# Kernel optimization log

Measured on AMD Instinct MI355X. Metric: run time of the kernel, lower is better.

## Reference

```python
import jax, jax.numpy as jnp
import numpy as np

D_MODEL = 512
N_HEADS = 12
EPS = 1e-5
_DIM = D_MODEL // N_HEADS          # 42
_REM = D_MODEL % N_HEADS           # 8
HEAD_DIMS = [_DIM + 1 if i < _REM else _DIM for i in range(N_HEADS)]  # sums to 512


def _layernorm(x, gamma, beta):
    mu = jnp.mean(x, axis=-1, keepdims=True)
    var = jnp.mean((x - mu) ** 2, axis=-1, keepdims=True)
    return (x - mu) * jax.lax.rsqrt(var + EPS) * gamma + beta


def setup_inputs() -> dict:
    key = jax.random.key(0)
    ks = jax.random.split(key, 12)
    S, B, D = 2048, 16, D_MODEL
    sc = 0.02
    return {
        "x":   jax.random.normal(ks[0], (S, B, D), jnp.float32),
        "Wq":  jax.random.normal(ks[1], (D, D), jnp.float32) * sc,
        "Wk":  jax.random.normal(ks[2], (D, D), jnp.float32) * sc,
        "Wv":  jax.random.normal(ks[3], (D, D), jnp.float32) * sc,
        "g1":  jnp.ones((D,), jnp.float32),
        "b1":  jnp.zeros((D,), jnp.float32),
        "g2":  jnp.ones((D,), jnp.float32),
        "b2":  jnp.zeros((D,), jnp.float32),
        "W_ffn1": jax.random.normal(ks[4], (D, D), jnp.float32) * sc,
        "b_ffn1": jnp.zeros((D,), jnp.float32),
        "W_ffn2": jax.random.normal(ks[5], (D, D), jnp.float32) * sc,
        "b_ffn2": jnp.zeros((D,), jnp.float32),
    }


def reference(x, Wq, Wk, Wv, g1, b1, g2, b2, W_ffn1, b_ffn1, W_ffn2, b_ffn2):
    # x: [S, B, D]; attention over S, batched over B (per source transpose [1,0,2])
    normed = _layernorm(x, g1, b1)
    q = jnp.transpose(normed @ Wq, (1, 0, 2))  # [B, S, D]
    k = jnp.transpose(normed @ Wk, (1, 0, 2))
    v = jnp.transpose(normed @ Wv, (1, 0, 2))

    outs = []
    idx = 0
    for hd in HEAD_DIMS:  # fixed small loop over structurally-distinct head dims
        q_i = q[:, :, idx:idx + hd]
        k_i = k[:, :, idx:idx + hd]
        v_i = v[:, :, idx:idx + hd]
        scores = jnp.einsum('bsd,btd->bst', q_i, k_i) / np.float32(np.sqrt(hd))
        attn = jax.nn.softmax(scores, axis=-1)  # dropout off (inference)
        outs.append(jnp.transpose(attn @ v_i, (1, 0, 2)))  # back to [S, B, hd]
        idx += hd

    attn_out = _layernorm(jnp.concatenate(outs, axis=-1) + x, g2, b2)
    ffn = jax.nn.relu(attn_out @ W_ffn1 + b_ffn1) @ W_ffn2 + b_ffn2
    return attn_out + ffn
```

## Files before the change

### kernel.cpp

```cpp
#include <hip/hip_runtime.h>
#include <hip/hip_bf16.h>


#define M_ROWS 32768
#define DM 512
#define SEQ 2048
#define BATCH 16
#define SLAB_ELEMS (24u * 1024u * 1024u)

typedef __bf16 bf16x8 __attribute__((ext_vector_type(8)));
typedef float f32x4 __attribute__((ext_vector_type(4)));
typedef float f32x16 __attribute__((ext_vector_type(16)));

#define EXP2F(x) __builtin_amdgcn_exp2f(x)

typedef __attribute__((address_space(3))) unsigned lds_u32;
typedef __attribute__((address_space(1))) unsigned glb_u32;
#define GL2LDS(src, dst) __builtin_amdgcn_global_load_lds( \
    (const glb_u32*)(const void*)(src), (lds_u32*)(void*)(dst), 16, 0, 0)

#define BARRIER_VM4() asm volatile("s_waitcnt vmcnt(4)\ns_barrier" ::: "memory")
#define BARRIER_VM2() asm volatile("s_waitcnt vmcnt(2)\ns_barrier" ::: "memory")
#define BARRIER_VM0() asm volatile("s_waitcnt vmcnt(0)\ns_barrier" ::: "memory")
#define BARRIER_ONLY() asm volatile("s_barrier" ::: "memory")

#define MFMA16(a, b, c) __builtin_amdgcn_mfma_f32_16x16x32_bf16(a, b, c, 0, 0, 0)

__device__ inline unsigned pkbf16(float a, float b) {
    unsigned r;
    asm("v_cvt_pk_bf16_f32 %0, %1, %2" : "=v"(r) : "v"(a), "v"(b));
    return r;
}

__global__ __launch_bounds__(256) void prep_kernel(
    const float* __restrict__ Wq, const float* __restrict__ Wk,
    const float* __restrict__ Wv, const float* __restrict__ Wf1,
    const float* __restrict__ Wf2, __bf16* __restrict__ Wts,
    __bf16* __restrict__ q, __bf16* __restrict__ v,
    const float* __restrict__ x, const float* __restrict__ g1,
    const float* __restrict__ b1, __bf16* __restrict__ normed)
{
    int blk = blockIdx.x;
    if (blk < 5120) {
        int g = blk >> 10;
        int idx = (blk & 1023) * 256 + threadIdx.x;
        const float* W = (g == 0) ? Wq : (g == 1) ? Wk : (g == 2) ? Wv
                        : (g == 3) ? Wf1 : Wf2;
        __bf16* Wt = Wts + (size_t)g * (DM * DM);
        int n = idx >> 9, k = idx & 511;
        Wt[idx] = (__bf16)W[k * DM + n];
    } else if (blk < 6656) {
        int row = (blk - 5120) * 256 + threadIdx.x;
        union { __bf16 h[8]; bf16x8 v8; } z;
#pragma unroll
        for (int j = 0; j < 8; ++j) z.h[j] = (__bf16)0.f;
        *(bf16x8*)(q + (size_t)row * 64 + 40) = z.v8;
    } else if (blk < 6848) {
        int i = (blk - 6656) * 256 + threadIdx.x;
        int bh = i >> 8, s8 = i & 255;
        int hd = ((bh % 12) < 8) ? 43 : 42;
        union { __bf16 h[8]; bf16x8 v8; } o;
#pragma unroll
        for (int j = 0; j < 8; ++j) o.h[j] = (__bf16)1.0f;
        *(bf16x8*)(v + ((size_t)bh * 64 + hd) * SEQ + s8 * 8) = o.v8;
    } else {
        int wid  = (int)(((blk - 6848) * 256 + threadIdx.x) >> 6);
        int lane = threadIdx.x & 63;
        int bb = wid >> 11, ss = wid & 2047;
        const float* xrow = x + ((size_t)ss * 16 + bb) * DM;
        float vv[8];
        *(float4*)&vv[0] = *(const float4*)(xrow + lane * 8);
        *(float4*)&vv[4] = *(const float4*)(xrow + lane * 8 + 4);
        float s = 0.f, sq = 0.f;
#pragma unroll
        for (int j = 0; j < 8; ++j) { s += vv[j]; sq = fmaf(vv[j], vv[j], sq); }
#pragma unroll
        for (int i = 1; i < 64; i <<= 1) { s += __shfl_xor(s, i); sq += __shfl_xor(sq, i); }
        float mu   = s * (1.0f / 512.0f);
        float var  = sq * (1.0f / 512.0f) - mu * mu;
        float rstd = rsqrtf(var + 1e-5f);
        union { __bf16 h[8]; bf16x8 v8; } o;
#pragma unroll
        for (int j = 0; j < 8; ++j)
            o.h[j] = (__bf16)((vv[j] - mu) * rstd * g1[lane * 8 + j] + b1[lane * 8 + j]);
        *(bf16x8*)(normed + (size_t)wid * DM + lane * 8) = o.v8;
    }
}

__global__ __launch_bounds__(256) void ln2_kernel(
    const __bf16* __restrict__ in, const float* __restrict__ res,
    const float* __restrict__ g, const float* __restrict__ b,
    __bf16* __restrict__ outb)
{
    int wid  = (int)((blockIdx.x * 256 + threadIdx.x) >> 6);
    int lane = threadIdx.x & 63;
    int bb = wid >> 11, ss = wid & 2047;
    union { __bf16 h[8]; bf16x8 v8; } iv;
    iv.v8 = *(const bf16x8*)(in + (size_t)wid * DM + lane * 8);
    const float* rrow = res + ((size_t)ss * 16 + bb) * DM;
    float v[8];
    float4 r0 = *(const float4*)(rrow + lane * 8);
    float4 r1 = *(const float4*)(rrow + lane * 8 + 4);
    v[0] = (float)iv.h[0] + r0.x; v[1] = (float)iv.h[1] + r0.y;
    v[2] = (float)iv.h[2] + r0.z; v[3] = (float)iv.h[3] + r0.w;
    v[4] = (float)iv.h[4] + r1.x; v[5] = (float)iv.h[5] + r1.y;
    v[6] = (float)iv.h[6] + r1.z; v[7] = (float)iv.h[7] + r1.w;
    float s = 0.f, sq = 0.f;
#pragma unroll
    for (int j = 0; j < 8; ++j) { s += v[j]; sq = fmaf(v[j], v[j], sq); }
#pragma unroll
    for (int i = 1; i < 64; i <<= 1) { s += __shfl_xor(s, i); sq += __shfl_xor(sq, i); }
    float mu   = s * (1.0f / 512.0f);
    float var  = sq * (1.0f / 512.0f) - mu * mu;
    float rstd = rsqrtf(var + 1e-5f);
    union { __bf16 h[8]; bf16x8 v8; } ob;
#pragma unroll
    for (int j = 0; j < 8; ++j)
        ob.h[j] = (__bf16)((v[j] - mu) * rstd * g[lane * 8 + j] + b[lane * 8 + j]);
    *(bf16x8*)(outb + (size_t)wid * DM + lane * 8) = ob.v8;
}

__global__ __launch_bounds__(512, 2) void gemm256_kernel(
    const __bf16* __restrict__ A, const __bf16* __restrict__ Wt,
    const float* __restrict__ bias, const __bf16* __restrict__ residb,
    void* __restrict__ Cout, int mode, int do_relu)
{
    extern __shared__ char lds[];
    const int tid  = threadIdx.x;
    const int lane = tid & 63, wave = tid >> 6;
    const int wm = wave >> 2, wn = wave & 3;
    const int m0 = blockIdx.y * 256, n0 = blockIdx.x * 256;
    if (mode == -1) {
        mode = 1 + blockIdx.z;
        Wt += (size_t)blockIdx.z * DM * DM;
        Cout = (void*)((__bf16*)Cout + (size_t)blockIdx.z * SLAB_ELEMS);
    }

    const int c0 = tid >> 4, r0 = tid & 15;
    const int rowoff = (c0 >> 2) * 16 + r0;
    const int kcol   = (c0 & 3) * 8;
    const __bf16* aS0 = A  + (size_t)(m0 + rowoff) * DM + kcol;
    const __bf16* aS1 = aS0 + (size_t)128 * DM;
    const __bf16* bS0 = Wt + (size_t)(n0 + rowoff) * DM + kcol;
    const __bf16* bS1 = bS0 + (size_t)128 * DM;

#define STG(tile, hh, buf) do { \
    const int kk_ = (tile) * 64 + ((hh) >> 1) * 32; \
    char* d_ = lds + (buf) * 65536 + ((hh) & 1) * 32768 + ((hh) >> 1) * 16384 + tid * 16; \
    const __bf16* sA_ = ((hh) & 1) ? bS0 : aS0; \
    const __bf16* sB_ = ((hh) & 1) ? bS1 : aS1; \
    GL2LDS(sA_ + kk_, d_); \
    GL2LDS(sB_ + kk_, d_ + 8192); \
} while (0)

    const int aRd = wm * 8192 + (lane >> 4) * 256 + (lane & 15) * 16;
    const int bRd = 32768 + wn * 4096 + (lane >> 4) * 256 + (lane & 15) * 16;

    f32x4 acc[8][4];
#pragma unroll
    for (int m = 0; m < 8; ++m)
#pragma unroll
        for (int n = 0; n < 4; ++n) acc[m][n] = f32x4{0.f, 0.f, 0.f, 0.f};

    STG(0, 0, 0); STG(0, 1, 0); STG(0, 2, 0); STG(0, 3, 0);
    BARRIER_VM4();

    bf16x8 bq0, bq1, bq2, bq3;

#define DO_PHASE(PH) do { \
    constexpr int buf_ = (PH) >> 2, kh_ = ((PH) >> 1) & 1, qm_ = (PH) & 1; \
    if constexpr ((PH) == 0) { if (it != 0) BARRIER_VM4(); } \
    else if constexpr (((PH) & 1) == 0) { \
        if (it == 3) BARRIER_VM0(); else BARRIER_VM4(); \
    } \
    char* base_ = lds + buf_ * 65536 + kh_ * 16384; \
    bf16x8 af0 = *(const bf16x8*)(base_ + aRd + (qm_ * 4 + 0) * 1024); \
    bf16x8 af1 = *(const bf16x8*)(base_ + aRd + (qm_ * 4 + 1) * 1024); \
    bf16x8 af2 = *(const bf16x8*)(base_ + aRd + (qm_ * 4 + 2) * 1024); \
    bf16x8 af3 = *(const bf16x8*)(base_ + aRd + (qm_ * 4 + 3) * 1024); \
    if constexpr (qm_ == 0) { \
        bq0 = *(const bf16x8*)(base_ + bRd + 0 * 1024); \
        bq1 = *(const bf16x8*)(base_ + bRd + 1 * 1024); \
        bq2 = *(const bf16x8*)(base_ + bRd + 2 * 1024); \
        bq3 = *(const bf16x8*)(base_ + bRd + 3 * 1024); \
    } \
    if constexpr ((PH) < 4) { STG(2 * it + 1, (PH), 1); } \
    else { if (it < 3) STG(2 * it + 2, (PH) - 4, 0); } \
    __builtin_amdgcn_s_setprio(1); \
    acc[qm_ * 4 + 0][0] = MFMA16(af0, bq0, acc[qm_ * 4 + 0][0]); \
    acc[qm_ * 4 + 0][1] = MFMA16(af0, bq1, acc[qm_ * 4 + 0][1]); \
    acc[qm_ * 4 + 0][2] = MFMA16(af0, bq2, acc[qm_ * 4 + 0][2]); \
    acc[qm_ * 4 + 0][3] = MFMA16(af0, bq3, acc[qm_ * 4 + 0][3]); \
    acc[qm_ * 4 + 1][0] = MFMA16(af1, bq0, acc[qm_ * 4 + 1][0]); \
    acc[qm_ * 4 + 1][1] = MFMA16(af1, bq1, acc[qm_ * 4 + 1][1]); \
    acc[qm_ * 4 + 1][2] = MFMA16(af1, bq2, acc[qm_ * 4 + 1][2]); \
    acc[qm_ * 4 + 1][3] = MFMA16(af1, bq3, acc[qm_ * 4 + 1][3]); \
    acc[qm_ * 4 + 2][0] = MFMA16(af2, bq0, acc[qm_ * 4 + 2][0]); \
    acc[qm_ * 4 + 2][1] = MFMA16(af2, bq1, acc[qm_ * 4 + 2][1]); \
    acc[qm_ * 4 + 2][2] = MFMA16(af2, bq2, acc[qm_ * 4 + 2][2]); \
    acc[qm_ * 4 + 2][3] = MFMA16(af2, bq3, acc[qm_ * 4 + 2][3]); \
    acc[qm_ * 4 + 3][0] = MFMA16(af3, bq0, acc[qm_ * 4 + 3][0]); \
    acc[qm_ * 4 + 3][1] = MFMA16(af3, bq1, acc[qm_ * 4 + 3][1]); \
    acc[qm_ * 4 + 3][2] = MFMA16(af3, bq2, acc[qm_ * 4 + 3][2]); \
    acc[qm_ * 4 + 3][3] = MFMA16(af3, bq3, acc[qm_ * 4 + 3][3]); \
    __builtin_amdgcn_s_setprio(0); \
} while (0)

    for (int it = 0; it < 4; ++it) {
        DO_PHASE(0); DO_PHASE(1); DO_PHASE(2); DO_PHASE(3);
        DO_PHASE(4); DO_PHASE(5); DO_PHASE(6); DO_PHASE(7);
    }
#undef DO_PHASE
#undef STG

#pragma unroll
    for (int m = 0; m < 8; ++m) {
#pragma unroll
        for (int n = 0; n < 4; ++n) {
            int col = n0 + wn * 64 + n * 16 + (lane & 15);
            int h = 0, d = 0;
            float sc = 1.f;
            if (mode >= 1 && mode <= 3) {
                if (col < 344) { h = col / 43; d = col - 43 * h; }
                else { int nn = col - 344; h = 8 + nn / 42; d = nn - 42 * (nn / 42); }
                if (mode == 1) sc = (h < 8) ? 0.22000894f : 0.22261268f;
            }
#pragma unroll
            for (int reg = 0; reg < 4; ++reg) {
                int row = m0 + wm * 128 + m * 16 + (lane >> 4) * 4 + reg;
                int b_ = row >> 11, s_ = row & 2047;
                float vv = acc[m][n][reg];
                if (bias) vv += bias[col];
                if (do_relu) vv = fmaxf(vv, 0.f);
                if (mode == 5) {
                    vv += (float)residb[(size_t)row * DM + col];
                    ((float*)Cout)[((size_t)s_ * 16 + b_) * DM + col] = vv;
                } else if (mode == 4) {
                    ((__bf16*)Cout)[(size_t)row * DM + col] = (__bf16)vv;
                } else {
                    if (mode == 1)
                        ((__bf16*)Cout)[(((size_t)b_ * 12 + h) * SEQ + s_) * 64 + d] = (__bf16)(vv * sc);
                    else if (mode == 2)
                        ((__bf16*)Cout)[(((size_t)b_ * 12 + h) * SEQ + s_) * 64 + d] = (__bf16)vv;
                    else
                        ((__bf16*)Cout)[(((size_t)b_ * 12 + h) * 64 + d) * SEQ + s_] = (__bf16)vv;
                }
            }
        }
    }
}

__global__ __launch_bounds__(256, 4) void attn_mfma_kernel(
    const __bf16* __restrict__ q, const __bf16* __restrict__ k,
    const __bf16* __restrict__ v, __bf16* __restrict__ attnc)
{
    __shared__ union {
        struct { __bf16 K[3][4096]; __bf16 V[2][4096]; } s;
        float Olds[4][32][33];
    } sm;
    char* smb = (char*)&sm;

    const int tid  = threadIdx.x;
    const int wave = tid >> 6, lane = tid & 63;
    const int ln = lane & 31, hi = lane >> 5;

    int sw = (blockIdx.x & 7) * 384 + (blockIdx.x >> 3);
    int qc = sw & 15;
    int h  = (sw >> 4) % 12;
    int b  = sw / 192;
    int hd  = (h < 8) ? 43 : 42;
    int off = (h < 8) ? 43 * h : 42 * h + 8;

    const __bf16* Qbh = q + ((size_t)b * 12 + h) * SEQ * 64;
    const char* Kbase = (const char*)(k + ((size_t)b * 12 + h) * SEQ * 64);
    const char* Vbase = (const char*)(v + ((size_t)b * 12 + h) * 64 * SEQ);

    int q0 = qc * 128 + wave * 32;

    bf16x8 qf[3];
#pragma unroll
    for (int ks = 0; ks < 3; ++ks)
        qf[ks] = *(const bf16x8*)(Qbh + (size_t)(q0 + ln) * 64 + ks * 16 + hi * 8);

    const int rc = tid >> 3;
    const int ob = (tid & 7) << 4;
    const int sb = ob ^ ((rc & 7) << 4);

#define STAGE_K(t, buf) do { \
    char* kd = smb + (buf) * 8192; \
    GL2LDS(Kbase + (size_t)(t) * 8192 + rc * 128 + sb,        kd + tid * 16); \
    GL2LDS(Kbase + (size_t)(t) * 8192 + rc * 128 + sb + 4096, kd + tid * 16 + 4096); \
} while (0)
#define STAGE_V(t, buf) do { \
    char* vd = smb + 24576 + (buf) * 8192; \
    GL2LDS(Vbase + (size_t)rc * 4096 + (t) * 128 + sb,        vd + tid * 16); \
    GL2LDS(Vbase + (size_t)(rc + 32) * 4096 + (t) * 128 + sb, vd + tid * 16 + 4096); \
} while (0)

    f32x16 oT0, oT1, z16;
#pragma unroll
    for (int i = 0; i < 16; ++i) { oT0[i] = 0.f; oT1[i] = 0.f; z16[i] = 0.f; }

    const int swr = (ln & 7) << 4;

    STAGE_K(0, 0);
    STAGE_V(0, 0);
    STAGE_K(1, 1);
    BARRIER_VM2();

#define DO_STACK(KROW, KSA0) do { \
    f32x16 s_; \
    __builtin_amdgcn_s_setprio(1); \
    { \
        int cb = (hi * 16) ^ swr; \
        bf16x8 ka = *(const bf16x8*)(Kc + (size_t)((KROW) + ln) * 64 + (cb >> 1)); \
        s_ = __builtin_amdgcn_mfma_f32_32x32x16_bf16(ka, qf[0], z16, 0, 0, 0); \
    } \
    { \
        int cb = (32 + hi * 16) ^ swr; \
        bf16x8 ka = *(const bf16x8*)(Kc + (size_t)((KROW) + ln) * 64 + (cb >> 1)); \
        s_ = __builtin_amdgcn_mfma_f32_32x32x16_bf16(ka, qf[1], s_, 0, 0, 0); \
    } \
    { \
        int cb = (64 + hi * 16) ^ swr; \
        bf16x8 ka = *(const bf16x8*)(Kc + (size_t)((KROW) + ln) * 64 + (cb >> 1)); \
        s_ = __builtin_amdgcn_mfma_f32_32x32x16_bf16(ka, qf[2], s_, 0, 0, 0); \
    } \
    __builtin_amdgcn_s_setprio(0); \
    _Pragma("unroll") \
    for (int i = 0; i < 16; ++i) s_[i] = EXP2F(s_[i]); \
    _Pragma("unroll") \
    for (int h16 = 0; h16 < 2; ++h16) { \
        const int pb = h16 * 8; \
        unsigned a0 = pkbf16(s_[pb + 0], s_[pb + 1]); \
        unsigned b0 = pkbf16(s_[pb + 4], s_[pb + 5]); \
        unsigned a1 = pkbf16(s_[pb + 2], s_[pb + 3]); \
        unsigned b1 = pkbf16(s_[pb + 6], s_[pb + 7]); \
        asm("v_permlane32_swap_b32 %0, %1" : "+v"(b0), "+v"(a0)); \
        asm("v_permlane32_swap_b32 %0, %1" : "+v"(b1), "+v"(a1)); \
        union { unsigned u[4]; bf16x8 v8; } bw; \
        bw.u[0] = a0; bw.u[1] = a1; bw.u[2] = b0; bw.u[3] = b1; \
        const int ksa = (KSA0) + h16; \
        int cb = (ksa * 32 + hi * 16) ^ swr; \
        __builtin_amdgcn_s_setprio(1); \
        bf16x8 va0 = *(const bf16x8*)(Vc + ln * 64 + (cb >> 1)); \
        bf16x8 va1 = *(const bf16x8*)(Vc + (ln + 32) * 64 + (cb >> 1)); \
        oT0 = __builtin_amdgcn_mfma_f32_32x32x16_bf16(va0, bw.v8, oT0, 0, 0, 0); \
        oT1 = __builtin_amdgcn_mfma_f32_32x32x16_bf16(va1, bw.v8, oT1, 0, 0, 0); \
        __builtin_amdgcn_s_setprio(0); \
    } \
} while (0)

    for (int t = 0; t < 32; ++t) {
        const int kb_ = t % 3, vb_ = t & 1;
        if (t < 31) STAGE_V(t + 1, (t + 1) & 1);
        if (t < 30) STAGE_K(t + 2, (t + 2) % 3);
        const __bf16* Kc = (const __bf16*)(smb + kb_ * 8192);
        const __bf16* Vc = (const __bf16*)(smb + 24576 + vb_ * 8192);

        DO_STACK(0, 0);
        DO_STACK(32, 2);

        if (t < 30)       BARRIER_VM2();
        else if (t == 30) BARRIER_VM0();
        else              BARRIER_ONLY();
    }
#undef DO_STACK
#undef STAGE_K
#undef STAGE_V

    float ls = (h < 8) ? oT1[7] : oT1[6];
    float lsp = __shfl_xor(ls, 32);
    float rl = 1.f / (hi ? lsp : ls);

    const int qr = lane & 31, ch = lane >> 5;
#pragma unroll
    for (int r = 0; r < 16; ++r) {
        int d0 = (r & 3) + 8 * (r >> 2) + 4 * hi;
        sm.Olds[wave][ln][d0] = oT0[r] * rl;
    }
    __syncthreads();
    {
        const float* row = &sm.Olds[wave][qr][ch * 16];
        __bf16* dst = attnc + ((size_t)b * SEQ + q0 + qr) * DM + off + ch * 16;
#pragma unroll
        for (int j = 0; j < 16; ++j) dst[j] = (__bf16)row[j];
    }
    __syncthreads();
#pragma unroll
    for (int r = 0; r < 16; ++r) {
        int d0 = (r & 3) + 8 * (r >> 2) + 4 * hi;
        sm.Olds[wave][ln][d0] = oT1[r] * rl;
    }
    __syncthreads();
    {
        const float* row = &sm.Olds[wave][qr][ch * 16];
        __bf16* dst = attnc + ((size_t)b * SEQ + q0 + qr) * DM + off + 32 + ch * 16;
        int lim = hd - 32 - ch * 16;
#pragma unroll
        for (int j = 0; j < 16; ++j)
            if (j < lim) dst[j] = (__bf16)row[j];
    }
}

extern "C" void kernel_launch(void* const* d_in, const int* in_sizes, int n_in,
                              void* d_out, int out_size, void* d_ws, size_t ws_size,
                              hipStream_t stream)
{
    const float* x   = (const float*)d_in[0];
    const float* Wq  = (const float*)d_in[1];
    const float* Wk  = (const float*)d_in[2];
    const float* Wv  = (const float*)d_in[3];
    const float* g1  = (const float*)d_in[4];
    const float* b1  = (const float*)d_in[5];
    const float* g2  = (const float*)d_in[6];
    const float* b2  = (const float*)d_in[7];
    const float* Wf1 = (const float*)d_in[8];
    const float* bf1 = (const float*)d_in[9];
    const float* Wf2 = (const float*)d_in[10];
    const float* bf2 = (const float*)d_in[11];
    float* out = (float*)d_out;

    const size_t MB = 1024 * 1024;
    if (ws_size < 208 * MB) return;
    char* ws = (char*)d_ws;
    __bf16* Wts  = (__bf16*)(ws);
    __bf16* Wf1t = Wts + 3 * DM * DM;
    __bf16* Wf2t = Wts + 4 * DM * DM;
    __bf16* normed_bf = (__bf16*)(ws + 4 * MB);
    __bf16* qb = (__bf16*)(ws + 36 * MB);
    __bf16* kb = (__bf16*)(ws + 84 * MB);
    __bf16* vb = (__bf16*)(ws + 132 * MB);
    __bf16* attnc = normed_bf;
    __bf16* attn_out_bf = (__bf16*)(ws + 100 * MB);
    __bf16* h1          = (__bf16*)(ws + 132 * MB);

    hipFuncSetAttribute((const void*)gemm256_kernel,
                        hipFuncAttributeMaxDynamicSharedMemorySize, 131072);

    dim3 gg(2, 128);
    dim3 gqkv(2, 128, 3);

    prep_kernel<<<15040, 256, 0, stream>>>(Wq, Wk, Wv, Wf1, Wf2, Wts, qb, vb,
                                           x, g1, b1, normed_bf);
    gemm256_kernel<<<gqkv, 512, 131072, stream>>>(normed_bf, Wts, nullptr, nullptr, qb, -1, 0);
    attn_mfma_kernel<<<BATCH * 12 * (SEQ / 128), 256, 0, stream>>>(qb, kb, vb, attnc);
    ln2_kernel<<<M_ROWS / 4, 256, 0, stream>>>(attnc, x, g2, b2, attn_out_bf);
    gemm256_kernel<<<gg, 512, 131072, stream>>>(attn_out_bf, Wf1t, bf1, nullptr, h1, 4, 1);
    gemm256_kernel<<<gg, 512, 131072, stream>>>(h1, Wf2t, bf2, attn_out_bf, out, 5, 0);
}
```

Before: 497.3 us.

## Double attention query tile to 256 per block and flatten QKV GEMM grid

The attention kernel now runs 512-thread blocks covering 256 queries, so each staged K/V tile feeds eight waves instead of four. This halves K/V global-to-LDS traffic per query, and each thread now issues a single load per stage. The QKV GEMM folds the Q/K/V selector from blockIdx.z into blockIdx.x so the three projections of the same row block are scheduled next to each other, which should improve L2 reuse of the activations. The GEMM's final-iteration full vmcnt wait is relaxed for the early phases. The risk is the raised launch-bounds occupancy target on attention, which limits registers per thread and may cause spills.

```diff
diff --git a/kernel.cpp b/kernel.cpp
--- a/kernel.cpp
+++ b/kernel.cpp
@@ -20,7 +20,7 @@
     (const glb_u32*)(const void*)(src), (lds_u32*)(void*)(dst), 16, 0, 0)
 
 #define BARRIER_VM4() asm volatile("s_waitcnt vmcnt(4)\ns_barrier" ::: "memory")
-#define BARRIER_VM2() asm volatile("s_waitcnt vmcnt(2)\ns_barrier" ::: "memory")
+#define BARRIER_VM1() asm volatile("s_waitcnt vmcnt(1)\ns_barrier" ::: "memory")
 #define BARRIER_VM0() asm volatile("s_waitcnt vmcnt(0)\ns_barrier" ::: "memory")
 #define BARRIER_ONLY() asm volatile("s_barrier" ::: "memory")
 
@@ -129,11 +129,16 @@
     const int tid  = threadIdx.x;
     const int lane = tid & 63, wave = tid >> 6;
     const int wm = wave >> 2, wn = wave & 3;
-    const int m0 = blockIdx.y * 256, n0 = blockIdx.x * 256;
+    const int m0 = blockIdx.y * 256;
+    int n0;
     if (mode == -1) {
-        mode = 1 + blockIdx.z;
-        Wt += (size_t)blockIdx.z * DM * DM;
-        Cout = (void*)((__bf16*)Cout + (size_t)blockIdx.z * SLAB_ELEMS);
+        int z = blockIdx.x >> 1;
+        mode = 1 + z;
+        Wt += (size_t)z * DM * DM;
+        Cout = (void*)((__bf16*)Cout + (size_t)z * SLAB_ELEMS);
+        n0 = (blockIdx.x & 1) * 256;
+    } else {
+        n0 = blockIdx.x * 256;
     }
 
     const int c0 = tid >> 4, r0 = tid & 15;
@@ -171,7 +176,7 @@
     constexpr int buf_ = (PH) >> 2, kh_ = ((PH) >> 1) & 1, qm_ = (PH) & 1; \
     if constexpr ((PH) == 0) { if (it != 0) BARRIER_VM4(); } \
     else if constexpr (((PH) & 1) == 0) { \
-        if (it == 3) BARRIER_VM0(); else BARRIER_VM4(); \
+        if (it == 3 && (PH) >= 4) BARRIER_VM0(); else BARRIER_VM4(); \
     } \
     char* base_ = lds + buf_ * 65536 + kh_ * 16384; \
     bf16x8 af0 = *(const bf16x8*)(base_ + aRd + (qm_ * 4 + 0) * 1024); \
@@ -250,13 +255,13 @@
     }
 }
 
-__global__ __launch_bounds__(256, 4) void attn_mfma_kernel(
+__global__ __launch_bounds__(512, 5) void attn_mfma_kernel(
     const __bf16* __restrict__ q, const __bf16* __restrict__ k,
     const __bf16* __restrict__ v, __bf16* __restrict__ attnc)
 {
     __shared__ union {
         struct { __bf16 K[3][4096]; __bf16 V[2][4096]; } s;
-        float Olds[4][32][33];
+        float Olds[8][32][33];
     } sm;
     char* smb = (char*)&sm;
 
@@ -264,10 +269,10 @@
     const int wave = tid >> 6, lane = tid & 63;
     const int ln = lane & 31, hi = lane >> 5;
 
-    int sw = (blockIdx.x & 7) * 384 + (blockIdx.x >> 3);
-    int qc = sw & 15;
-    int h  = (sw >> 4) % 12;
-    int b  = sw / 192;
+    int sw = (blockIdx.x & 7) * 192 + (blockIdx.x >> 3);
+    int qc = sw & 7;
+    int h  = (sw >> 3) % 12;
+    int b  = sw / 96;
     int hd  = (h < 8) ? 43 : 42;
     int off = (h < 8) ? 43 * h : 42 * h + 8;
 
@@ -275,7 +280,7 @@
     const char* Kbase = (const char*)(k + ((size_t)b * 12 + h) * SEQ * 64);
     const char* Vbase = (const char*)(v + ((size_t)b * 12 + h) * 64 * SEQ);
 
-    int q0 = qc * 128 + wave * 32;
+    int q0 = qc * 256 + wave * 32;
 
     bf16x8 qf[3];
 #pragma unroll
@@ -286,16 +291,10 @@
     const int ob = (tid & 7) << 4;
     const int sb = ob ^ ((rc & 7) << 4);
 
-#define STAGE_K(t, buf) do { \
-    char* kd = smb + (buf) * 8192; \
-    GL2LDS(Kbase + (size_t)(t) * 8192 + rc * 128 + sb,        kd + tid * 16); \
-    GL2LDS(Kbase + (size_t)(t) * 8192 + rc * 128 + sb + 4096, kd + tid * 16 + 4096); \
-} while (0)
-#define STAGE_V(t, buf) do { \
-    char* vd = smb + 24576 + (buf) * 8192; \
-    GL2LDS(Vbase + (size_t)rc * 4096 + (t) * 128 + sb,        vd + tid * 16); \
-    GL2LDS(Vbase + (size_t)(rc + 32) * 4096 + (t) * 128 + sb, vd + tid * 16 + 4096); \
-} while (0)
+#define STAGE_K(t, buf) \
+    GL2LDS(Kbase + (size_t)(t) * 8192 + rc * 128 + sb, smb + (buf) * 8192 + tid * 16)
+#define STAGE_V(t, buf) \
+    GL2LDS(Vbase + (size_t)rc * 4096 + (t) * 128 + sb, smb + 24576 + (buf) * 8192 + tid * 16)
 
     f32x16 oT0, oT1, z16;
 #pragma unroll
@@ -306,7 +305,7 @@
     STAGE_K(0, 0);
     STAGE_V(0, 0);
     STAGE_K(1, 1);
-    BARRIER_VM2();
+    BARRIER_VM1();
 
 #define DO_STACK(KROW, KSA0) do { \
     f32x16 s_; \
@@ -361,7 +360,7 @@
         DO_STACK(0, 0);
         DO_STACK(32, 2);
 
-        if (t < 30)       BARRIER_VM2();
+        if (t < 30)       BARRIER_VM1();
         else if (t == 30) BARRIER_VM0();
         else              BARRIER_ONLY();
     }
@@ -439,12 +438,12 @@
                         hipFuncAttributeMaxDynamicSharedMemorySize, 131072);
 
     dim3 gg(2, 128);
-    dim3 gqkv(2, 128, 3);
+    dim3 gqkv(6, 128);
 
     prep_kernel<<<15040, 256, 0, stream>>>(Wq, Wk, Wv, Wf1, Wf2, Wts, qb, vb,
                                            x, g1, b1, normed_bf);
     gemm256_kernel<<<gqkv, 512, 131072, stream>>>(normed_bf, Wts, nullptr, nullptr, qb, -1, 0);
-    attn_mfma_kernel<<<BATCH * 12 * (SEQ / 128), 256, 0, stream>>>(qb, kb, vb, attnc);
+    attn_mfma_kernel<<<BATCH * 12 * (SEQ / 256), 512, 0, stream>>>(qb, kb, vb, attnc);
     ln2_kernel<<<M_ROWS / 4, 256, 0, stream>>>(attnc, x, g2, b2, attn_out_bf);
     gemm256_kernel<<<gg, 512, 131072, stream>>>(attn_out_bf, Wf1t, bf1, nullptr, h1, 4, 1);
     gemm256_kernel<<<gg, 512, 131072, stream>>>(h1, Wf2t, bf2, attn_out_bf, out, 5, 0);
```

New measurement: 504.4 us. About the same (+1.4%).
